# Kernel tuning notes

Hardware: AMD Instinct MI355X
Metric: run time of the kernel (lower is better)

The kernel has to match this reference:

```python
import jax, jax.numpy as jnp
import numpy as np

N = 50000          # nodes
E = 3_200_000      # edges (radius-graph topology, avg degree ~64)
C = 10             # node channels
ED = 4             # edge_dim: [dist, dx, dy, food_flag]
H = 16             # message hidden dim
RADIUS = 0.05
ACC_SCALE = 0.005
MAX_VEL = 0.02
EDGES_TO_STAY_ALIVE = 3
CONSUMPTION_EDGES_REQUIRED = 3
NOISE_SCALE = 0.004


def setup_inputs() -> dict:
    key = jax.random.key(0)
    ks = jax.random.split(key, 10)
    pos = jax.random.uniform(ks[0], (N, 2), minval=-1.0, maxval=1.0)
    vel = jax.random.uniform(ks[1], (N, 2), minval=-MAX_VEL, maxval=MAX_VEL)
    # column 4: 1.0 = living cell, 0.0 = food node
    is_cell = (jax.random.uniform(ks[2], (N,)) > 0.2).astype(jnp.float32)
    hidden = jax.random.normal(ks[3], (N, C - 5)) * 0.1
    x = jnp.concatenate([pos, vel, is_cell[:, None], hidden], axis=1)  # [N,10]
    src = jax.random.randint(ks[4], (E,), 0, N)
    dst = jax.random.randint(ks[5], (E,), 0, N)
    noise = jax.random.uniform(ks[6], (N, 2))  # uniform [0,1), mapped to [-1,1) inside
    W_edge = jax.random.normal(ks[7], (ED, H)) * 0.3
    W_src = jax.random.normal(ks[8], (C, H)) * 0.3
    b1 = jnp.zeros((H,), jnp.float32)
    W_out = jax.random.normal(ks[9], (H, 4)) * 0.3
    b2 = jnp.zeros((4,), jnp.float32)
    return dict(x=x, src=src, dst=dst, noise=noise, W_edge=W_edge,
                W_src=W_src, b1=b1, W_out=W_out, b2=b2)


def reference(x, src, dst, noise, W_edge, W_src, b1, W_out, b2):
    pos = x[:, :2]
    vel = x[:, 2:4]
    cell = x[:, 4]
    c_mask = (cell == 1.0).astype(x.dtype)          # [N]

    # ---- edge attributes of the (dynamic) radius graph ----
    d = pos[src] - pos[dst]                          # [E,2] gather
    dist = jnp.sqrt(jnp.sum(d * d, axis=1) + 1e-12)  # [E]
    food_flag = cell[src]                            # 0 for food-source edges
    edge_attr = jnp.concatenate([dist[:, None], d, food_flag[:, None]], axis=1)  # [E,4]

    # ---- message passing: per-edge MLP + scatter-sum + node readout ----
    m = jax.nn.relu(edge_attr @ W_edge + x[src] @ W_src + b1)     # [E,H]
    agg = jax.ops.segment_sum(m, dst, num_segments=N)             # [N,H]
    h = jnp.tanh(agg @ W_out + b2) * c_mask[:, None]              # [N,4], masked as in update_graph

    # ---- velocity / position update ----
    acc = h[:, :2] * ACC_SCALE
    new_vel = jnp.clip(vel + acc, -MAX_VEL, MAX_VEL)
    new_pos = pos + new_vel                                       # wrap_around = False
    vel_noisy = new_vel + (noise * 2.0 - 1.0) * NOISE_SCALE * c_mask[:, None]
    new_x = jnp.concatenate(
        [new_pos, vel_noisy, cell[:, None], h[:, 2:], x[:, 7:]], axis=1)  # [N,10]

    # ---- costs / stats ----
    eps = 1e-6
    border_mask = (jnp.abs(new_pos) > 1.0).astype(x.dtype)        # [N,2]
    border_cost = jnp.sum(jnp.log(jnp.abs(new_pos) + eps) * border_mask)
    food_edge = (food_flag == 0.0)
    visible_food = food_edge.sum()
    mean_food_dist = jnp.sum(dist * food_edge.astype(x.dtype))

    # ---- node removal masks (jit-safe: return keep mask instead of slicing) ----
    deg = jax.ops.segment_sum(jnp.ones_like(dist), dst, num_segments=N)
    dead = (cell == 1.0) & (deg < EDGES_TO_STAY_ALIVE)
    consume_e = (dist < RADIUS) & (cell[src] == 1.0) & (cell[dst] == 0.0)
    cdeg = jax.ops.segment_sum(consume_e.astype(x.dtype), dst, num_segments=N)
    consumed = (cell == 0.0) & (cdeg >= CONSUMPTION_EDGES_REQUIRED)
    keep_mask = ~(dead | consumed)

    velocity_bonus = jnp.mean(jnp.abs(new_vel), axis=0)           # [2]
    dead_cost = dead.sum()
    food_reward = consumed.sum()
    return (new_x, keep_mask, velocity_bonus, border_cost, food_reward,
            dead_cost, visible_food, mean_food_dist)
```

## Files before the change

kernel.cpp:

```cpp
#include <hip/hip_runtime.h>
#include <math.h>

#define NN 50000
#define NE 3200000

#define NT    98
#define TSZ   512
#define CAP   34816
#define SCB   625
#define EPB   5120
#define EPT   20
#define NSL   8

static constexpr float ACC_SCALE   = 0.005f;
static constexpr float MAX_VEL     = 0.02f;
static constexpr float NOISE_SCALE = 0.004f;
static constexpr float RADIUS      = 0.05f;

#define OUT_KEEP   500000
#define OUT_SCAL   550000

#define WS_NI    0
#define WS_S2    200704
#define WS_GCUR  1003520
#define WS_BK    1005120
#define WS_PACC  4417088
#define WS_PDEG  6022720

__global__ __launch_bounds__(256) void k1_prep(
    const float* __restrict__ x,
    const float* __restrict__ W_edge,
    const float* __restrict__ W_src,
    const float* __restrict__ b1,
    float4* __restrict__ nodeinfo,
    float* __restrict__ s2,
    int* __restrict__ gcur,
    float* __restrict__ out_scalars)
{
    int n = blockIdx.x * 256 + threadIdx.x;
    if (blockIdx.x == 0) {
        if (threadIdx.x < 7) out_scalars[threadIdx.x] = 0.0f;
        for (int i = threadIdx.x; i < NT * 16; i += 256)
            gcur[i] = (i & 15) ? 0 : (i >> 4) * CAP;
    }
    if (n >= NN) return;

    float xr[10];
#pragma unroll
    for (int c = 0; c < 10; ++c) xr[c] = x[n * 10 + c];
    float cell = xr[4];

    nodeinfo[n] = make_float4(xr[0], xr[1], cell, 0.0f);

#pragma unroll
    for (int j = 0; j < 16; ++j) {
        float v = fmaf(cell, W_edge[48 + j], b1[j]);
#pragma unroll
        for (int c = 0; c < 10; ++c) v = fmaf(xr[c], W_src[c * 16 + j], v);
        s2[n * 16 + j] = v;
    }
}

__global__ __launch_bounds__(256) void k_scatter(
    const int* __restrict__ src,
    const int* __restrict__ dst,
    int* __restrict__ gcur,
    unsigned* __restrict__ bucket)
{
    __shared__ unsigned      stage[EPB];
    __shared__ unsigned char binid[EPB];
    __shared__ int hist[NT], binstart[NT], lcur[NT], gbase[NT];
    __shared__ int scanbuf[128];

    int tid = threadIdx.x;
    for (int i = tid; i < NT; i += 256) { hist[i] = 0; lcur[i] = 0; }
    __syncthreads();

    int e0 = blockIdx.x * EPB;

    int d[EPT];
#pragma unroll
    for (int j = 0; j < EPT; ++j) d[j] = dst[e0 + j * 256 + tid];
#pragma unroll
    for (int j = 0; j < EPT; ++j) atomicAdd(&hist[d[j] >> 9], 1);
    __syncthreads();

    if (tid < 128) scanbuf[tid] = (tid < NT) ? hist[tid] : 0;
    __syncthreads();
    for (int off = 1; off < 128; off <<= 1) {
        int v = 0;
        if (tid < 128 && tid >= off) v = scanbuf[tid - off];
        __syncthreads();
        if (tid < 128) scanbuf[tid] += v;
        __syncthreads();
    }
    if (tid < NT) {
        binstart[tid] = scanbuf[tid] - hist[tid];
        gbase[tid] = atomicAdd(&gcur[tid * 16], hist[tid]);
    }
    __syncthreads();

    int sreg[EPT];
#pragma unroll
    for (int j = 0; j < EPT; ++j) sreg[j] = src[e0 + j * 256 + tid];
#pragma unroll
    for (int j = 0; j < EPT; ++j) {
        int t = d[j] >> 9;
        int pos = binstart[t] + atomicAdd(&lcur[t], 1);
        stage[pos] = (unsigned)sreg[j] | ((unsigned)(d[j] & 511) << 16);
        binid[pos] = (unsigned char)t;
    }
    __syncthreads();

#pragma unroll
    for (int j = 0; j < EPT; ++j) {
        int i = j * 256 + tid;
        int b = binid[i];
        int g = gbase[b] + (i - binstart[b]);
        if (g < (b + 1) * CAP) bucket[g] = stage[i];
    }
}

__global__ __launch_bounds__(512) void k_agg(
    const float* __restrict__ W_edge,
    const float* __restrict__ W_out,
    const float4* __restrict__ nodeinfo,
    const float* __restrict__ s2,
    const int* __restrict__ gcur,
    const unsigned* __restrict__ bucket,
    float4* __restrict__ pacc,
    int* __restrict__ pdeg,
    float* __restrict__ out_scalars)
{
    __shared__ float  sAcc[TSZ][4];
    __shared__ int    sDeg[TSZ];
    __shared__ float4 sNI[TSZ];
    __shared__ float  sRed[8][2];

    int t   = blockIdx.x >> 3;
    int sl  = blockIdx.x & 7;
    int tid = threadIdx.x;

    for (int j = tid; j < TSZ; j += 512) {
        int g = t * TSZ + j;
        sNI[j] = (g < NN) ? nodeinfo[g] : make_float4(9e9f, 9e9f, -1.f, 0.f);
        sAcc[j][0] = 0.f; sAcc[j][1] = 0.f; sAcc[j][2] = 0.f; sAcc[j][3] = 0.f;
        sDeg[j] = 0;
    }

    float w0[16], w1[16], w2[16], woa[16], wob[16], woc[16], wod[16];
#pragma unroll
    for (int k = 0; k < 16; ++k) {
        w0[k] = W_edge[k];
        w1[k] = W_edge[16 + k];
        w2[k] = W_edge[32 + k];
        woa[k] = W_out[k * 4 + 0];
        wob[k] = W_out[k * 4 + 1];
        woc[k] = W_out[k * 4 + 2];
        wod[k] = W_out[k * 4 + 3];
    }
    __syncthreads();

    int cnt = gcur[t * 16] - t * CAP;
    if (cnt > CAP) cnt = CAP;
    int cs = (cnt + NSL - 1) / NSL;
    int i0 = sl * cs;
    int i1 = min(i0 + cs, cnt);

    float vis = 0.f, fd = 0.f;
#pragma unroll 2
    for (int i = i0 + tid; i < i1; i += 512) {
        unsigned e = bucket[t * CAP + i];
        int s  = e & 0xFFFF;
        int dl = (e >> 16) & 0x1FF;
        float4 ns = nodeinfo[s];
        float4 nt = sNI[dl];
        float dx = ns.x - nt.x;
        float dy = ns.y - nt.y;
        float dist = sqrtf(fmaf(dx, dx, fmaf(dy, dy, 1e-12f)));

        bool food0 = (ns.z == 0.0f);
        vis += food0 ? 1.f : 0.f;
        fd  += food0 ? dist : 0.f;

        bool consume = (dist < RADIUS) && (ns.z == 1.0f) && (nt.z == 0.0f);
        atomicAdd(&sDeg[dl], consume ? 65537 : 1);

        const float4* sv4 = (const float4*)(s2 + (size_t)s * 16);
        float4 q0 = sv4[0], q1 = sv4[1], q2 = sv4[2], q3 = sv4[3];
        float sv[16] = { q0.x, q0.y, q0.z, q0.w, q1.x, q1.y, q1.z, q1.w,
                         q2.x, q2.y, q2.z, q2.w, q3.x, q3.y, q3.z, q3.w };

        float v0 = 0.f, v1 = 0.f, v2 = 0.f, v3 = 0.f;
#pragma unroll
        for (int k = 0; k < 16; ++k) {
            float m = fmaf(dist, w0[k], fmaf(dx, w1[k], fmaf(dy, w2[k], sv[k])));
            m = fmaxf(m, 0.0f);
            v0 = fmaf(m, woa[k], v0);
            v1 = fmaf(m, wob[k], v1);
            v2 = fmaf(m, woc[k], v2);
            v3 = fmaf(m, wod[k], v3);
        }
        atomicAdd(&sAcc[dl][0], v0);
        atomicAdd(&sAcc[dl][1], v1);
        atomicAdd(&sAcc[dl][2], v2);
        atomicAdd(&sAcc[dl][3], v3);
    }
    __syncthreads();

    for (int j = tid; j < TSZ; j += 512) {
        int o = sl * (NT * TSZ) + t * TSZ + j;
        pacc[o] = make_float4(sAcc[j][0], sAcc[j][1], sAcc[j][2], sAcc[j][3]);
        pdeg[o] = sDeg[j];
    }

#pragma unroll
    for (int off = 32; off > 0; off >>= 1) {
        vis += __shfl_down(vis, off);
        fd  += __shfl_down(fd,  off);
    }
    int lane = tid & 63, wv = tid >> 6;
    if (lane == 0) { sRed[wv][0] = vis; sRed[wv][1] = fd; }
    __syncthreads();
    if (tid == 0) {
        float a = 0.f, b = 0.f;
#pragma unroll
        for (int wq = 0; wq < 8; ++wq) { a += sRed[wq][0]; b += sRed[wq][1]; }
        atomicAdd(&out_scalars[5], a);
        atomicAdd(&out_scalars[6], b);
    }
}

__global__ __launch_bounds__(256) void k_final(
    const float* __restrict__ x,
    const float* __restrict__ noise,
    const float* __restrict__ b2,
    const float4* __restrict__ pacc,
    const int* __restrict__ pdeg,
    float* __restrict__ out,
    float* __restrict__ out_scalars)
{
    __shared__ float sRed[4][5];
    int n = blockIdx.x * 256 + threadIdx.x;
    int tid = threadIdx.x;

    float avx = 0.f, avy = 0.f, bc = 0.f, deadf = 0.f, consf = 0.f;

    if (n < NN) {
        float a0 = 0.f, a1 = 0.f, a2 = 0.f, a3 = 0.f;
        int dp = 0;
#pragma unroll
        for (int sl = 0; sl < NSL; ++sl) {
            float4 q = pacc[sl * (NT * TSZ) + n];
            a0 += q.x; a1 += q.y; a2 += q.z; a3 += q.w;
            dp += pdeg[sl * (NT * TSZ) + n];
        }

        float cell = x[n * 10 + 4];
        float cm = (cell == 1.0f) ? 1.0f : 0.0f;
        float h0 = tanhf(a0 + b2[0]) * cm;
        float h1 = tanhf(a1 + b2[1]) * cm;
        float h2 = tanhf(a2 + b2[2]) * cm;
        float h3 = tanhf(a3 + b2[3]) * cm;

        float px = x[n * 10 + 0], py = x[n * 10 + 1];
        float vx = x[n * 10 + 2], vy = x[n * 10 + 3];

        float nvx = fminf(fmaxf(fmaf(h0, ACC_SCALE, vx), -MAX_VEL), MAX_VEL);
        float nvy = fminf(fmaxf(fmaf(h1, ACC_SCALE, vy), -MAX_VEL), MAX_VEL);
        float npx = px + nvx;
        float npy = py + nvy;

        float vnx = nvx + (noise[n * 2 + 0] * 2.0f - 1.0f) * NOISE_SCALE * cm;
        float vny = nvy + (noise[n * 2 + 1] * 2.0f - 1.0f) * NOISE_SCALE * cm;

        float* row = out + (size_t)n * 10;
        row[0] = npx;  row[1] = npy;
        row[2] = vnx;  row[3] = vny;
        row[4] = cell; row[5] = h2;  row[6] = h3;
        row[7] = x[n * 10 + 7];
        row[8] = x[n * 10 + 8];
        row[9] = x[n * 10 + 9];

        float apx = fabsf(npx), apy = fabsf(npy);
        if (apx > 1.0f) bc += logf(apx + 1e-6f);
        if (apy > 1.0f) bc += logf(apy + 1e-6f);

        int deg  = dp & 0xFFFF;
        int cdeg = dp >> 16;
        bool dead = (cell == 1.0f) && (deg < 3);
        bool cons = (cell == 0.0f) && (cdeg >= 3);
        out[OUT_KEEP + n] = (dead || cons) ? 0.0f : 1.0f;
        deadf = dead ? 1.0f : 0.0f;
        consf = cons ? 1.0f : 0.0f;
        avx = fabsf(nvx) * (1.0f / NN);
        avy = fabsf(nvy) * (1.0f / NN);
    }

    float r[5] = { avx, avy, bc, consf, deadf };
#pragma unroll
    for (int q = 0; q < 5; ++q) {
#pragma unroll
        for (int off = 32; off > 0; off >>= 1)
            r[q] += __shfl_down(r[q], off);
    }
    int lane = tid & 63, wv = tid >> 6;
    if (lane == 0) {
#pragma unroll
        for (int q = 0; q < 5; ++q) sRed[wv][q] = r[q];
    }
    __syncthreads();
    if (tid == 0) {
#pragma unroll
        for (int q = 0; q < 5; ++q) {
            float acc = sRed[0][q] + sRed[1][q] + sRed[2][q] + sRed[3][q];
            atomicAdd(&out_scalars[q], acc);
        }
    }
}

extern "C" void kernel_launch(void* const* d_in, const int* in_sizes, int n_in,
                              void* d_out, int out_size, void* d_ws, size_t ws_size,
                              hipStream_t stream) {
    const float* x      = (const float*)d_in[0];
    const int*   src    = (const int*)  d_in[1];
    const int*   dst    = (const int*)  d_in[2];
    const float* noise  = (const float*)d_in[3];
    const float* W_edge = (const float*)d_in[4];
    const float* W_src  = (const float*)d_in[5];
    const float* b1     = (const float*)d_in[6];
    const float* W_out  = (const float*)d_in[7];
    const float* b2     = (const float*)d_in[8];

    float* ws = (float*)d_ws;
    float4*   nodeinfo = (float4*)(ws + WS_NI);
    float*    s2       = ws + WS_S2;
    int*      gcur     = (int*)(ws + WS_GCUR);
    unsigned* bucket   = (unsigned*)(ws + WS_BK);
    float4*   pacc     = (float4*)(ws + WS_PACC);
    int*      pdeg     = (int*)(ws + WS_PDEG);

    float* out         = (float*)d_out;
    float* out_scalars = out + OUT_SCAL;

    k1_prep<<<196, 256, 0, stream>>>(
        x, W_edge, W_src, b1, nodeinfo, s2, gcur, out_scalars);

    k_scatter<<<SCB, 256, 0, stream>>>(src, dst, gcur, bucket);

    k_agg<<<NT * NSL, 512, 0, stream>>>(
        W_edge, W_out, nodeinfo, s2, gcur, bucket, pacc, pdeg, out_scalars);

    k_final<<<196, 256, 0, stream>>>(
        x, noise, b2, pacc, pdeg, out, out_scalars);
}
```

Before: 220.3 us.

## Prefetch next edge in aggregation, shrink blocks, widen slicing, pack scatter bin ids

```diff
diff --git a/kernel.cpp b/kernel.cpp
--- a/kernel.cpp
+++ b/kernel.cpp
@@ -7,10 +7,9 @@
 #define NT    98
 #define TSZ   512
 #define CAP   34816
-#define SCB   625
-#define EPB   5120
-#define EPT   20
-#define NSL   8
+#define SCB   1250
+#define EPB   2560
+#define EPT   10
 
 static constexpr float ACC_SCALE   = 0.005f;
 static constexpr float MAX_VEL     = 0.02f;
@@ -25,7 +24,6 @@
 #define WS_GCUR  1003520
 #define WS_BK    1005120
 #define WS_PACC  4417088
-#define WS_PDEG  6022720
 
 __global__ __launch_bounds__(256) void k1_prep(
     const float* __restrict__ x,
@@ -33,7 +31,7 @@
     const float* __restrict__ W_src,
     const float* __restrict__ b1,
     float4* __restrict__ nodeinfo,
-    float* __restrict__ s2,
+    float4* __restrict__ s2,
     int* __restrict__ gcur,
     float* __restrict__ out_scalars)
 {
@@ -52,13 +50,17 @@
 
     nodeinfo[n] = make_float4(xr[0], xr[1], cell, 0.0f);
 
+    float v[16];
 #pragma unroll
     for (int j = 0; j < 16; ++j) {
-        float v = fmaf(cell, W_edge[48 + j], b1[j]);
-#pragma unroll
-        for (int c = 0; c < 10; ++c) v = fmaf(xr[c], W_src[c * 16 + j], v);
-        s2[n * 16 + j] = v;
-    }
+        float a = fmaf(cell, W_edge[48 + j], b1[j]);
+#pragma unroll
+        for (int c = 0; c < 10; ++c) a = fmaf(xr[c], W_src[c * 16 + j], a);
+        v[j] = a;
+    }
+#pragma unroll
+    for (int q = 0; q < 4; ++q)
+        s2[(size_t)n * 4 + q] = make_float4(v[q*4], v[q*4+1], v[q*4+2], v[q*4+3]);
 }
 
 __global__ __launch_bounds__(256) void k_scatter(
@@ -67,8 +69,7 @@
     int* __restrict__ gcur,
     unsigned* __restrict__ bucket)
 {
-    __shared__ unsigned      stage[EPB];
-    __shared__ unsigned char binid[EPB];
+    __shared__ unsigned stage[EPB];
     __shared__ int hist[NT], binstart[NT], lcur[NT], gbase[NT];
     __shared__ int scanbuf[128];
 
@@ -95,8 +96,9 @@
         __syncthreads();
     }
     if (tid < NT) {
-        binstart[tid] = scanbuf[tid] - hist[tid];
-        gbase[tid] = atomicAdd(&gcur[tid * 16], hist[tid]);
+        int bs = scanbuf[tid] - hist[tid];
+        binstart[tid] = bs;
+        gbase[tid] = atomicAdd(&gcur[tid * 16], hist[tid]) - bs;
     }
     __syncthreads();
 
@@ -107,21 +109,22 @@
     for (int j = 0; j < EPT; ++j) {
         int t = d[j] >> 9;
         int pos = binstart[t] + atomicAdd(&lcur[t], 1);
-        stage[pos] = (unsigned)sreg[j] | ((unsigned)(d[j] & 511) << 16);
-        binid[pos] = (unsigned char)t;
+        stage[pos] = (unsigned)sreg[j] | ((unsigned)(d[j] & 511) << 16)
+                   | ((unsigned)t << 25);
     }
     __syncthreads();
 
 #pragma unroll
     for (int j = 0; j < EPT; ++j) {
         int i = j * 256 + tid;
-        int b = binid[i];
-        int g = gbase[b] + (i - binstart[b]);
-        if (g < (b + 1) * CAP) bucket[g] = stage[i];
-    }
-}
-
-__global__ __launch_bounds__(512) void k_agg(
+        unsigned e = stage[i];
+        int b = e >> 25;
+        int g = gbase[b] + i;
+        if (g < (b + 1) * CAP) bucket[g] = e;
+    }
+}
+
+__global__ __launch_bounds__(256, 6) void k_agg(
     const float* __restrict__ W_edge,
     const float* __restrict__ W_out,
     const float4* __restrict__ nodeinfo,
@@ -130,20 +133,23 @@
     const unsigned* __restrict__ bucket,
     float4* __restrict__ pacc,
     int* __restrict__ pdeg,
-    float* __restrict__ out_scalars)
+    float* __restrict__ out_scalars,
+    int lg)
 {
-    __shared__ float  sAcc[TSZ][4];
-    __shared__ int    sDeg[TSZ];
-    __shared__ float4 sNI[TSZ];
-    __shared__ float  sRed[8][2];
-
-    int t   = blockIdx.x >> 3;
-    int sl  = blockIdx.x & 7;
+    __shared__ float sAcc[TSZ][5];
+    __shared__ int   sDeg[TSZ];
+    __shared__ float sPX[TSZ], sPY[TSZ], sCL[TSZ];
+    __shared__ float sRed[4][2];
+
+    int t   = blockIdx.x >> lg;
+    int sl  = blockIdx.x & ((1 << lg) - 1);
+    int nsl = 1 << lg;
     int tid = threadIdx.x;
 
-    for (int j = tid; j < TSZ; j += 512) {
+    for (int j = tid; j < TSZ; j += 256) {
         int g = t * TSZ + j;
-        sNI[j] = (g < NN) ? nodeinfo[g] : make_float4(9e9f, 9e9f, -1.f, 0.f);
+        float4 ni = (g < NN) ? nodeinfo[g] : make_float4(9e9f, 9e9f, -1.f, 0.f);
+        sPX[j] = ni.x; sPY[j] = ni.y; sCL[j] = ni.z;
         sAcc[j][0] = 0.f; sAcc[j][1] = 0.f; sAcc[j][2] = 0.f; sAcc[j][3] = 0.f;
         sDeg[j] = 0;
     }
@@ -163,34 +169,44 @@
 
     int cnt = gcur[t * 16] - t * CAP;
     if (cnt > CAP) cnt = CAP;
-    int cs = (cnt + NSL - 1) / NSL;
+    int cs = (cnt + nsl - 1) / nsl;
     int i0 = sl * cs;
     int i1 = min(i0 + cs, cnt);
 
+    const unsigned* bk = bucket + (size_t)t * CAP;
     float vis = 0.f, fd = 0.f;
-#pragma unroll 2
-    for (int i = i0 + tid; i < i1; i += 512) {
-        unsigned e = bucket[t * CAP + i];
-        int s  = e & 0xFFFF;
-        int dl = (e >> 16) & 0x1FF;
-        float4 ns = nodeinfo[s];
-        float4 nt = sNI[dl];
-        float dx = ns.x - nt.x;
-        float dy = ns.y - nt.y;
+
+    int i = i0 + tid;
+    int ic = min(i, i1 - 1); if (ic < 0) ic = 0;
+    unsigned eA = bk[ic];
+    int sA = eA & 0xFFFF;
+    float4 niA = nodeinfo[sA];
+    const float4* rA = (const float4*)(s2 + (size_t)sA * 16);
+    float4 a0 = rA[0], a1 = rA[1], a2 = rA[2], a3 = rA[3];
+
+    for (; i < i1; i += 256) {
+        int icn = min(i + 256, i1 - 1);
+        unsigned eB = bk[icn];
+        int sB = eB & 0xFFFF;
+        float4 niB = nodeinfo[sB];
+        const float4* rB = (const float4*)(s2 + (size_t)sB * 16);
+        float4 b0 = rB[0], b1v = rB[1], b2v = rB[2], b3v = rB[3];
+
+        int dl = (eA >> 16) & 0x1FF;
+        float dx = niA.x - sPX[dl];
+        float dy = niA.y - sPY[dl];
+        float ctl = sCL[dl];
         float dist = sqrtf(fmaf(dx, dx, fmaf(dy, dy, 1e-12f)));
 
-        bool food0 = (ns.z == 0.0f);
+        bool food0 = (niA.z == 0.0f);
         vis += food0 ? 1.f : 0.f;
         fd  += food0 ? dist : 0.f;
 
-        bool consume = (dist < RADIUS) && (ns.z == 1.0f) && (nt.z == 0.0f);
+        bool consume = (dist < RADIUS) && (niA.z == 1.0f) && (ctl == 0.0f);
         atomicAdd(&sDeg[dl], consume ? 65537 : 1);
 
-        const float4* sv4 = (const float4*)(s2 + (size_t)s * 16);
-        float4 q0 = sv4[0], q1 = sv4[1], q2 = sv4[2], q3 = sv4[3];
-        float sv[16] = { q0.x, q0.y, q0.z, q0.w, q1.x, q1.y, q1.z, q1.w,
-                         q2.x, q2.y, q2.z, q2.w, q3.x, q3.y, q3.z, q3.w };
-
+        float sv[16] = { a0.x, a0.y, a0.z, a0.w, a1.x, a1.y, a1.z, a1.w,
+                         a2.x, a2.y, a2.z, a2.w, a3.x, a3.y, a3.z, a3.w };
         float v0 = 0.f, v1 = 0.f, v2 = 0.f, v3 = 0.f;
 #pragma unroll
         for (int k = 0; k < 16; ++k) {
@@ -205,10 +221,12 @@
         atomicAdd(&sAcc[dl][1], v1);
         atomicAdd(&sAcc[dl][2], v2);
         atomicAdd(&sAcc[dl][3], v3);
-    }
-    __syncthreads();
-
-    for (int j = tid; j < TSZ; j += 512) {
+
+        eA = eB; niA = niB; a0 = b0; a1 = b1v; a2 = b2v; a3 = b3v;
+    }
+    __syncthreads();
+
+    for (int j = tid; j < TSZ; j += 256) {
         int o = sl * (NT * TSZ) + t * TSZ + j;
         pacc[o] = make_float4(sAcc[j][0], sAcc[j][1], sAcc[j][2], sAcc[j][3]);
         pdeg[o] = sDeg[j];
@@ -225,7 +243,7 @@
     if (tid == 0) {
         float a = 0.f, b = 0.f;
 #pragma unroll
-        for (int wq = 0; wq < 8; ++wq) { a += sRed[wq][0]; b += sRed[wq][1]; }
+        for (int wq = 0; wq < 4; ++wq) { a += sRed[wq][0]; b += sRed[wq][1]; }
         atomicAdd(&out_scalars[5], a);
         atomicAdd(&out_scalars[6], b);
     }
@@ -238,24 +256,31 @@
     const float4* __restrict__ pacc,
     const int* __restrict__ pdeg,
     float* __restrict__ out,
-    float* __restrict__ out_scalars)
+    float* __restrict__ out_scalars,
+    int nsl)
 {
     __shared__ float sRed[4][5];
-    int n = blockIdx.x * 256 + threadIdx.x;
-    int tid = threadIdx.x;
+    int tid  = threadIdx.x;
+    int n    = blockIdx.x * 128 + (tid >> 1);
+    int half = tid & 1;
+
+    float a0 = 0.f, a1 = 0.f, a2 = 0.f, a3 = 0.f;
+    int dp = 0;
+    if (n < NN) {
+        for (int sl = half; sl < nsl; sl += 2) {
+            float4 q = pacc[(size_t)sl * (NT * TSZ) + n];
+            a0 += q.x; a1 += q.y; a2 += q.z; a3 += q.w;
+            dp += pdeg[(size_t)sl * (NT * TSZ) + n];
+        }
+    }
+    a0 += __shfl_xor(a0, 1);
+    a1 += __shfl_xor(a1, 1);
+    a2 += __shfl_xor(a2, 1);
+    a3 += __shfl_xor(a3, 1);
+    dp += __shfl_xor(dp, 1);
 
     float avx = 0.f, avy = 0.f, bc = 0.f, deadf = 0.f, consf = 0.f;
-
-    if (n < NN) {
-        float a0 = 0.f, a1 = 0.f, a2 = 0.f, a3 = 0.f;
-        int dp = 0;
-#pragma unroll
-        for (int sl = 0; sl < NSL; ++sl) {
-            float4 q = pacc[sl * (NT * TSZ) + n];
-            a0 += q.x; a1 += q.y; a2 += q.z; a3 += q.w;
-            dp += pdeg[sl * (NT * TSZ) + n];
-        }
-
+    if (n < NN && half == 0) {
         float cell = x[n * 10 + 4];
         float cm = (cell == 1.0f) ? 1.0f : 0.0f;
         float h0 = tanhf(a0 + b2[0]) * cm;
@@ -332,25 +357,30 @@
     const float* W_out  = (const float*)d_in[7];
     const float* b2     = (const float*)d_in[8];
 
+    size_t need16 = ((size_t)WS_PACC + 16ull * NT * TSZ * 5) * 4;
+    int lg  = (ws_size >= need16) ? 4 : 3;
+    int nsl = 1 << lg;
+
     float* ws = (float*)d_ws;
     float4*   nodeinfo = (float4*)(ws + WS_NI);
     float*    s2       = ws + WS_S2;
     int*      gcur     = (int*)(ws + WS_GCUR);
     unsigned* bucket   = (unsigned*)(ws + WS_BK);
     float4*   pacc     = (float4*)(ws + WS_PACC);
-    int*      pdeg     = (int*)(ws + WS_PDEG);
+    int*      pdeg     = (int*)(ws + WS_PACC + (size_t)nsl * NT * TSZ * 4);
 
     float* out         = (float*)d_out;
     float* out_scalars = out + OUT_SCAL;
 
     k1_prep<<<196, 256, 0, stream>>>(
-        x, W_edge, W_src, b1, nodeinfo, s2, gcur, out_scalars);
+        x, W_edge, W_src, b1, nodeinfo, (float4*)s2, gcur, out_scalars);
 
     k_scatter<<<SCB, 256, 0, stream>>>(src, dst, gcur, bucket);
 
-    k_agg<<<NT * NSL, 512, 0, stream>>>(
-        W_edge, W_out, nodeinfo, s2, gcur, bucket, pacc, pdeg, out_scalars);
-
-    k_final<<<196, 256, 0, stream>>>(
-        x, noise, b2, pacc, pdeg, out, out_scalars);
-}
+    k_agg<<<NT * nsl, 256, 0, stream>>>(
+        W_edge, W_out, nodeinfo, s2, gcur, bucket, pacc, pdeg,
+        out_scalars, lg);
+
+    k_final<<<392, 256, 0, stream>>>(
+        x, noise, b2, pacc, pdeg, out, out_scalars, nsl);
+}
```

Result: slower. 243.7 us (+10.6%).
